# Kernel tuning notes

Hardware: AMD Instinct MI355X
Metric: run time of the kernel (lower is better)

The kernel has to match this reference:

```python
import jax, jax.numpy as jnp
import numpy as np

B, N, C, H, HD, HH, WW, K, ALPHA = 8, 4096, 256, 8, 32, 64, 64, 5, 4.0


def setup_inputs() -> dict:
    key = jax.random.key(0)
    ks = jax.random.split(key, 6)
    return {
        "x": jax.random.normal(ks[0], (B, N, C), jnp.float32),
        "W_qg": jax.random.normal(ks[1], (C, 2 * C), jnp.float32) * 0.02,
        "W_kv": jax.random.normal(ks[2], (C, 2 * C), jnp.float32) * 0.02,
        "W_proj": jax.random.normal(ks[3], (C, C), jnp.float32) * 0.02,
        "b_proj": jnp.zeros((C,), jnp.float32),
        "dwc_w": jax.random.normal(ks[4], (HD, 1, K, K), jnp.float32) * 0.05,
        "dwc_b": jnp.zeros((HD,), jnp.float32),
        "power_p": jnp.zeros((1, H, 1, HD), jnp.float32),
    }


def _safe_pow(x, p):
    # x >= 0 (post-relu). 0**p == 0 for p > 0; guard base so grads stay finite.
    xs = jnp.where(x > 0, x, 1.0)
    return jnp.where(x > 0, xs ** p, 0.0)


def reference(x, W_qg, W_kv, W_proj, b_proj, dwc_w, dwc_b, power_p):
    qg = x @ W_qg                                  # (B,N,2C)
    q, g = qg[..., :C], qg[..., C:]
    kv = x @ W_kv                                  # (B,N,2C)
    k = kv[..., :C].reshape(B, N, H, HD).transpose(0, 2, 1, 3)   # (B,H,N,hd)
    v = kv[..., C:].reshape(B, N, H, HD).transpose(0, 2, 1, 3)
    q = q.reshape(B, N, H, HD).transpose(0, 2, 1, 3)

    power = 1.0 + ALPHA * jax.nn.sigmoid(power_p)  # (1,H,1,hd)
    # x_s = q_pos@kv_s + q_neg@kv_s = (q_pos+q_neg)@kv_s, kv_s = (k_pos+k_neg)^T v_s
    q_sum = _safe_pow(jax.nn.relu(q), power) + _safe_pow(jax.nn.relu(-q), power)
    k_sum = _safe_pow(jax.nn.relu(k), power) + _safe_pow(jax.nn.relu(-k), power)

    v_s, v_o = v[..., : HD // 2], v[..., HD // 2 :]
    kv_s = jnp.einsum('bhnd,bhne->bhde', k_sum, v_s)
    kv_o = jnp.einsum('bhnd,bhne->bhde', k_sum, v_o)
    x_s = jnp.einsum('bhnd,bhde->bhne', q_sum, kv_s)
    x_o = jnp.einsum('bhnd,bhde->bhne', q_sum, kv_o)
    x_att = jnp.concatenate([x_s, x_o], -1).transpose(0, 2, 1, 3).reshape(B, N, C)

    # depthwise conv branch: exact layout replication of torch permute/reshape chain
    v_img = v.transpose(0, 2, 1, 3).reshape(B * H, HD, HH, WW)
    pad = K // 2
    v_loc = jax.lax.conv_general_dilated(
        v_img, dwc_w, (1, 1), [(pad, pad), (pad, pad)],
        feature_group_count=HD,
        dimension_numbers=('NCHW', 'OIHW', 'NCHW')) + dwc_b[None, :, None, None]
    v_loc = v_loc.reshape(B, H, HD, N).transpose(0, 2, 1, 3).reshape(B, C, N).transpose(0, 2, 1)

    return ((x_att + v_loc) * g) @ W_proj + b_proj
```

## Files before the change

### kernel.cpp

```cpp
#include <hip/hip_runtime.h>
#include <hip/hip_bf16.h>
#include <math.h>

#define B_ 8
#define N_ 4096
#define C_ 256
#define H_ 8
#define HD_ 32
#define BN_ (B_ * N_)
#define E_ ((size_t)BN_ * C_)

typedef __attribute__((ext_vector_type(8))) short short8;
typedef __attribute__((ext_vector_type(4))) float f32x4;

__device__ __forceinline__ float b2f(__hip_bfloat16 x) { return __bfloat162float(x); }

__device__ __forceinline__ void gl_lds16(const void* gp, void* lp) {
    __builtin_amdgcn_global_load_lds(
        (const __attribute__((address_space(1))) unsigned int*)gp,
        (__attribute__((address_space(3))) unsigned int*)lp,
        16, 0, 0);
}

__device__ __forceinline__ float fast_abspow(float v, float p) {
    float av = fabsf(v);
    return (av > 0.f) ? __builtin_amdgcn_exp2f(p * __builtin_amdgcn_logf(av)) : 0.f;
}

__device__ __forceinline__ float bf_lo(unsigned u) { return __uint_as_float(u << 16); }
__device__ __forceinline__ float bf_hi(unsigned u) { return __uint_as_float(u & 0xffff0000u); }
__device__ __forceinline__ unsigned short f2bfbits(float f) {
    __hip_bfloat16 h = __float2bfloat16(f);
    return *(unsigned short*)&h;
}
__device__ __forceinline__ unsigned pack2(float lo, float hi) {
    return (unsigned)f2bfbits(lo) | ((unsigned)f2bfbits(hi) << 16);
}

__global__ __launch_bounds__(256) void cvt_all(
    const float* __restrict__ x, const float* __restrict__ Wqg,
    const float* __restrict__ Wkv, const float* __restrict__ Wp,
    const float* __restrict__ pp,
    __hip_bfloat16* __restrict__ xb, __hip_bfloat16* __restrict__ Wt1,
    __hip_bfloat16* __restrict__ Wt2, float* __restrict__ powers,
    float* __restrict__ kv_mat2)
{
    int t = threadIdx.x;
    int bid0 = blockIdx.x;
    if (bid0 < 4096) {
        size_t i = ((size_t)bid0 * 256 + t) * 8;
        float4 a = *(const float4*)&x[i];
        float4 b = *(const float4*)&x[i + 4];
        uint4 o = {pack2(a.x, a.y), pack2(a.z, a.w), pack2(b.x, b.y), pack2(b.z, b.w)};
        *(uint4*)&xb[i] = o;
        return;
    }
    int bid = bid0 - 4096;
    if (bid == 80) {
        powers[t] = 1.0f + 4.0f / (1.0f + expf(-pp[t]));
        return;
    }
    if (bid >= 81) {
        ((float4*)kv_mat2)[(size_t)(bid - 81) * 256 + t] = (float4){0.f, 0.f, 0.f, 0.f};
        return;
    }
    __shared__ float tile[64][65];
    const float* src;
    __hip_bfloat16* dst;
    int scols, tr, tc, dn0;
    if (bid < 32)      { src = Wqg; scols = 512; tr = bid >> 3;        tc = bid & 7;        dst = Wt1; dn0 = tc * 64; }
    else if (bid < 64) { src = Wkv; scols = 512; tr = (bid - 32) >> 3; tc = (bid - 32) & 7; dst = Wt1; dn0 = 512 + tc * 64; }
    else               { src = Wp;  scols = 256; tr = (bid - 64) >> 2; tc = (bid - 64) & 3; dst = Wt2; dn0 = tc * 64; }
    int tx = t & 63, ty = t >> 6;
    #pragma unroll
    for (int i = 0; i < 16; i++) {
        int r = ty + i * 4;
        tile[r][tx] = src[(size_t)(tr * 64 + r) * scols + tc * 64 + tx];
    }
    __syncthreads();
    #pragma unroll
    for (int i = 0; i < 16; i++) {
        int n_local = ty + i * 4;
        dst[(size_t)(dn0 + n_local) * 256 + tr * 64 + tx] = __float2bfloat16(tile[tx][n_local]);
    }
}

__global__ __launch_bounds__(256) void gemm1_mfma(
    const __hip_bfloat16* __restrict__ xb, const __hip_bfloat16* __restrict__ Wt1,
    const float* __restrict__ powers,
    __hip_bfloat16* __restrict__ q16, __hip_bfloat16* __restrict__ k16,
    __hip_bfloat16* __restrict__ g16, __hip_bfloat16* __restrict__ v16)
{
    __shared__ __align__(16) unsigned short ABs[128 * 128];
    int t = threadIdx.x;
    int w = t >> 6, l = t & 63;
    int bswz = (blockIdx.x & 7) * 256 + (blockIdx.x >> 3);
    int row0 = (bswz >> 3) * 128;
    int colb = bswz & 7;
    int col0 = colb * 128;
    int wm = (w >> 1) * 64, wn = (w & 1) * 64;
    int lane15 = l & 15, quad = l >> 4;
    int srow4 = l >> 2;
    int sgc = ((l & 3) ^ ((l >> 3) & 3)) * 8;

    f32x4 acc[4][4];
    #pragma unroll
    for (int mi = 0; mi < 4; mi++)
        #pragma unroll
        for (int ni = 0; ni < 4; ni++) acc[mi][ni] = (f32x4){0.f, 0.f, 0.f, 0.f};

    #pragma unroll
    for (int j = 0; j < 2; j++) {
        int rowl = j * 64 + w * 16 + srow4;
        gl_lds16(&xb[(size_t)(row0 + rowl) * 256 + sgc],
                 &ABs[(j * 64 + w * 16) * 32]);
        gl_lds16(&Wt1[(size_t)(col0 + rowl) * 256 + sgc],
                 &ABs[8192 + (j * 64 + w * 16) * 32]);
    }
    __syncthreads();

    for (int ti = 0; ti < 8; ti++) {
        int cur = ti & 1;
        if (ti < 7) {
            int nxt = cur ^ 1;
            int kn = (ti + 1) * 32;
            #pragma unroll
            for (int j = 0; j < 2; j++) {
                int rowl = j * 64 + w * 16 + srow4;
                gl_lds16(&xb[(size_t)(row0 + rowl) * 256 + kn + sgc],
                         &ABs[nxt * 4096 + (j * 64 + w * 16) * 32]);
                gl_lds16(&Wt1[(size_t)(col0 + rowl) * 256 + kn + sgc],
                         &ABs[8192 + nxt * 4096 + (j * 64 + w * 16) * 32]);
            }
        }
        const unsigned short* Ac = ABs + cur * 4096;
        const unsigned short* Bc = ABs + 8192 + cur * 4096;
        short8 a[4], b[4];
        #pragma unroll
        for (int mi = 0; mi < 4; mi++) {
            int r = wm + mi * 16 + lane15;
            a[mi] = *(const short8*)&Ac[r * 32 + ((quad ^ ((r >> 1) & 3)) << 3)];
        }
        #pragma unroll
        for (int ni = 0; ni < 4; ni++) {
            int r = wn + ni * 16 + lane15;
            b[ni] = *(const short8*)&Bc[r * 32 + ((quad ^ ((r >> 1) & 3)) << 3)];
        }
        #pragma unroll
        for (int mi = 0; mi < 4; mi++)
            #pragma unroll
            for (int ni = 0; ni < 4; ni++)
                acc[mi][ni] = __builtin_amdgcn_mfma_f32_16x16x32_bf16(a[mi], b[ni], acc[mi][ni], 0, 0, 0);
        __syncthreads();
    }

    int region = colb >> 1;
    bool dopow = (region == 0) || (region == 2);
    __hip_bfloat16* dst = (region == 0) ? q16 : (region == 1) ? g16 : (region == 2) ? k16 : v16;
    int cbase = col0 & 255;
    #pragma unroll
    for (int mi = 0; mi < 4; mi++) {
        #pragma unroll
        for (int ni = 0; ni < 4; ni++) {
            int rowb = wm + mi * 16 + quad * 4;
            int coll = wn + ni * 16 + lane15;
            float p = powers[cbase + coll];
            int cchunk = coll >> 3, cin = coll & 7;
            #pragma unroll
            for (int r = 0; r < 4; r++) {
                int rl = rowb + r;
                float v = acc[mi][ni][r];
                float o = dopow ? fast_abspow(v, p) : v;
                ABs[rl * 128 + ((cchunk ^ (rl & 15)) << 3) + cin] = f2bfbits(o);
            }
        }
    }
    __syncthreads();
    #pragma unroll
    for (int j = 0; j < 8; j++) {
        int g = j * 256 + t;
        int rl = g >> 4, chunk = g & 15;
        uint4 vv = *(const uint4*)&ABs[rl * 128 + ((chunk ^ (rl & 15)) << 3)];
        *(uint4*)&dst[(size_t)(row0 + rl) * 256 + cbase + chunk * 8] = vv;
    }
}

__global__ __launch_bounds__(256) void kvconv_kernel(
    const __hip_bfloat16* __restrict__ k16, const __hip_bfloat16* __restrict__ v16,
    float* __restrict__ kv_mat2,
    const float* __restrict__ w, const float* __restrict__ bias,
    __hip_bfloat16* __restrict__ vloc)
{
    __shared__ __align__(16) unsigned char smraw[18560];
    int t = threadIdx.x;

    if (blockIdx.x < 512) {
        unsigned short (*KV)[32][136] = (unsigned short (*)[32][136])smraw;
        int w_ = t >> 6, l = t & 63;
        int lane15 = l & 15, quad = l >> 4;
        int bid = blockIdx.x;
        int pair = bid >> 3, seg = bid & 7;
        int b = pair >> 3, h = pair & 7;
        int nloc = t & 127, cs = (t >> 7) * 16;

        f32x4 acc[2][2];
        #pragma unroll
        for (int di = 0; di < 2; di++)
            #pragma unroll
            for (int ei = 0; ei < 2; ei++) acc[di][ei] = (f32x4){0.f, 0.f, 0.f, 0.f};

        const size_t base = (size_t)b * N_ * 256 + h * 32 + cs;
        for (int c4 = 0; c4 < 4; c4++) {
            int n0 = seg * 512 + c4 * 128;
            const uint4* kp = (const uint4*)(k16 + base + (size_t)(n0 + nloc) * 256);
            uint4 ka = kp[0], kb = kp[1];
            const uint4* vp = (const uint4*)(v16 + base + (size_t)(n0 + nloc) * 256);
            uint4 va = vp[0], vb = vp[1];
            __syncthreads();
            unsigned kw[8] = {ka.x, ka.y, ka.z, ka.w, kb.x, kb.y, kb.z, kb.w};
            unsigned vw[8] = {va.x, va.y, va.z, va.w, vb.x, vb.y, vb.z, vb.w};
            #pragma unroll
            for (int j = 0; j < 8; j++) {
                KV[0][cs + 2 * j][nloc]     = (unsigned short)(kw[j] & 0xffffu);
                KV[0][cs + 2 * j + 1][nloc] = (unsigned short)(kw[j] >> 16);
                KV[1][cs + 2 * j][nloc]     = (unsigned short)(vw[j] & 0xffffu);
                KV[1][cs + 2 * j + 1][nloc] = (unsigned short)(vw[j] >> 16);
            }
            __syncthreads();
            int nb = w_ * 32 + quad * 8;
            short8 a[2], bb[2];
            #pragma unroll
            for (int di = 0; di < 2; di++)
                a[di] = *(const short8*)&KV[0][di * 16 + lane15][nb];
            #pragma unroll
            for (int ei = 0; ei < 2; ei++)
                bb[ei] = *(const short8*)&KV[1][ei * 16 + lane15][nb];
            #pragma unroll
            for (int di = 0; di < 2; di++)
                #pragma unroll
                for (int ei = 0; ei < 2; ei++)
                    acc[di][ei] = __builtin_amdgcn_mfma_f32_16x16x32_bf16(a[di], bb[ei], acc[di][ei], 0, 0, 0);
        }

        __syncthreads();
        float* red = (float*)smraw;
        #pragma unroll
        for (int di = 0; di < 2; di++)
            #pragma unroll
            for (int ei = 0; ei < 2; ei++) {
                int e = ei * 16 + lane15;
                #pragma unroll
                for (int r = 0; r < 4; r++) {
                    int d = di * 16 + quad * 4 + r;
                    red[w_ * 1056 + e * 33 + d] = acc[di][ei][r];
                }
            }
        __syncthreads();
        #pragma unroll
        for (int j = 0; j < 4; j++) {
            int o = j * 256 + t;
            int e = o >> 5, d = o & 31;
            float s = red[e * 33 + d] + red[1056 + e * 33 + d]
                    + red[2112 + e * 33 + d] + red[3168 + e * 33 + d];
            atomicAdd(&kv_mat2[(size_t)b * 8192 + e * 256 + h * 32 + d], s);
        }
        return;
    }

    float* img = (float*)smraw;
    float* wl  = (float*)(smraw + 18432);
    int gid = blockIdx.x - 512;
    int DD = gid & 31;
    if (t < 128) {
        int row = t >> 1, side = (t & 1) * 68;
        *(float4*)&img[row * 72 + side] = (float4){0.f, 0.f, 0.f, 0.f};
    }
    if (t < 25) wl[t] = w[DD * 25 + t];
    {
        int row = t >> 2, colb = (t & 3) * 16;
        const uint4* src = (const uint4*)(v16 + (size_t)gid * 4096 + row * 64 + colb);
        uint4 u0 = src[0], u1 = src[1];
        float4* d = (float4*)&img[row * 72 + 4 + colb];
        d[0] = (float4){bf_lo(u0.x), bf_hi(u0.x), bf_lo(u0.y), bf_hi(u0.y)};
        d[1] = (float4){bf_lo(u0.z), bf_hi(u0.z), bf_lo(u0.w), bf_hi(u0.w)};
        d[2] = (float4){bf_lo(u1.x), bf_hi(u1.x), bf_lo(u1.y), bf_hi(u1.y)};
        d[3] = (float4){bf_lo(u1.z), bf_hi(u1.z), bf_lo(u1.w), bf_hi(u1.w)};
    }
    __syncthreads();
    float bs = bias[DD];
    int x0 = (t & 15) * 4, yb = t >> 4;
    #pragma unroll
    for (int s = 0; s < 4; s++) {
        int y = yb + s * 16;
        float a0 = bs, a1 = bs, a2 = bs, a3 = bs;
        #pragma unroll
        for (int ky = 0; ky < 5; ky++) {
            int row = y + ky - 2;
            if (row < 0 || row >= 64) continue;
            const float* rp = &img[row * 72 + x0];
            float4 w0 = *(const float4*)rp;
            float4 w1 = *(const float4*)(rp + 4);
            float4 w2 = *(const float4*)(rp + 8);
            float win[12] = {w0.x, w0.y, w0.z, w0.w, w1.x, w1.y, w1.z, w1.w,
                             w2.x, w2.y, w2.z, w2.w};
            #pragma unroll
            for (int kx = 0; kx < 5; kx++) {
                float wt = wl[ky * 5 + kx];
                a0 += wt * win[2 + kx];
                a1 += wt * win[3 + kx];
                a2 += wt * win[4 + kx];
                a3 += wt * win[5 + kx];
            }
        }
        unsigned lo = pack2(a0, a1);
        unsigned hi = pack2(a2, a3);
        *(uint2*)(vloc + (size_t)gid * 4096 + y * 64 + x0) = (uint2){lo, hi};
    }
}

#define A2P 264
__global__ __launch_bounds__(512) void att_gemm2(
    const __hip_bfloat16* __restrict__ q16, const float* __restrict__ kv_mat2,
    const __hip_bfloat16* __restrict__ vloc, const __hip_bfloat16* __restrict__ g16,
    const __hip_bfloat16* __restrict__ Wt2, const float* __restrict__ bp,
    float* __restrict__ out)
{
    __shared__ __align__(16) unsigned short QA[64 * A2P];
    __shared__ __align__(16) unsigned short Bs[256 * 32];
    int t = threadIdx.x;
    int w = t >> 6, l = t & 63;
    int r0 = blockIdx.x * 64;
    int b = r0 >> 12, n0 = r0 & 4095;
    int lane15 = l & 15, quad = l >> 4;
    int h = w;

    {
        const uint4* qsrc = (const uint4*)(q16 + (size_t)(r0 + (t >> 3)) * 256 + (t & 7) * 32);
        uint4* qdst = (uint4*)&QA[(t >> 3) * A2P + (t & 7) * 32];
        #pragma unroll
        for (int j = 0; j < 4; j++) qdst[j] = qsrc[j];
    }
    __syncthreads();

    short8 afr[4];
    #pragma unroll
    for (int m = 0; m < 4; m++)
        afr[m] = *(const short8*)&QA[(m * 16 + lane15) * A2P + h * 32 + quad * 8];

    short8 bfr[2];
    #pragma unroll
    for (int nt = 0; nt < 2; nt++) {
        const float4* kp = (const float4*)(kv_mat2 + (size_t)b * 8192 +
            (size_t)(nt * 16 + lane15) * 256 + h * 32 + quad * 8);
        float4 ka = kp[0], kb = kp[1];
        short8 bb;
        bb[0] = (short)f2bfbits(ka.x); bb[1] = (short)f2bfbits(ka.y);
        bb[2] = (short)f2bfbits(ka.z); bb[3] = (short)f2bfbits(ka.w);
        bb[4] = (short)f2bfbits(kb.x); bb[5] = (short)f2bfbits(kb.y);
        bb[6] = (short)f2bfbits(kb.z); bb[7] = (short)f2bfbits(kb.w);
        bfr[nt] = bb;
    }

    f32x4 ac[4][2];
    #pragma unroll
    for (int m = 0; m < 4; m++)
        #pragma unroll
        for (int nt = 0; nt < 2; nt++)
            ac[m][nt] = __builtin_amdgcn_mfma_f32_16x16x32_bf16(
                afr[m], bfr[nt], (f32x4){0.f, 0.f, 0.f, 0.f}, 0, 0, 0);

    #pragma unroll
    for (int m = 0; m < 4; m++) {
        #pragma unroll
        for (int nt = 0; nt < 2; nt++) {
            int col = h * 32 + nt * 16 + lane15;
            int rowb = m * 16 + quad * 4;
            size_t img = ((size_t)((b * 8 + (col & 7)) * 32 + (col >> 3))) * 4096 + n0 + rowb;
            uint2 vv = *(const uint2*)(vloc + img);
            float vl[4] = {bf_lo(vv.x), bf_hi(vv.x), bf_lo(vv.y), bf_hi(vv.y)};
            #pragma unroll
            for (int i = 0; i < 4; i++) {
                float gg = b2f(g16[(size_t)(r0 + rowb + i) * 256 + col]);
                float val = (ac[m][nt][i] + vl[i]) * gg;
                QA[(rowb + i) * A2P + col] = f2bfbits(val);
            }
        }
    }

    int wm = (w & 1) * 32, wn = (w >> 1) * 64;
    f32x4 acc2[2][4];
    #pragma unroll
    for (int mi = 0; mi < 2; mi++)
        #pragma unroll
        for (int ni = 0; ni < 4; ni++) acc2[mi][ni] = (f32x4){0.f, 0.f, 0.f, 0.f};

    for (int k0 = 0; k0 < 256; k0 += 32) {
        __syncthreads();
        #pragma unroll
        for (int j = 0; j < 2; j++) {
            int rowl = j * 128 + w * 16 + (l >> 2);
            int gchunk = (l & 3) ^ ((rowl >> 1) & 3);
            gl_lds16(&Wt2[(size_t)rowl * 256 + k0 + gchunk * 8],
                     &Bs[(j * 128 + w * 16) * 32]);
        }
        __syncthreads();
        short8 a[2], bb[4];
        #pragma unroll
        for (int mi = 0; mi < 2; mi++)
            a[mi] = *(const short8*)&QA[(wm + mi * 16 + lane15) * A2P + k0 + quad * 8];
        #pragma unroll
        for (int ni = 0; ni < 4; ni++) {
            int r = wn + ni * 16 + lane15;
            bb[ni] = *(const short8*)&Bs[r * 32 + ((quad ^ ((r >> 1) & 3)) << 3)];
        }
        #pragma unroll
        for (int mi = 0; mi < 2; mi++)
            #pragma unroll
            for (int ni = 0; ni < 4; ni++)
                acc2[mi][ni] = __builtin_amdgcn_mfma_f32_16x16x32_bf16(a[mi], bb[ni], acc2[mi][ni], 0, 0, 0);
    }

    #pragma unroll
    for (int mi = 0; mi < 2; mi++) {
        #pragma unroll
        for (int ni = 0; ni < 4; ni++) {
            int row = r0 + wm + mi * 16 + quad * 4;
            int col = wn + ni * 16 + lane15;
            float bv = bp[col];
            #pragma unroll
            for (int r = 0; r < 4; r++)
                out[(size_t)(row + r) * 256 + col] = acc2[mi][ni][r] + bv;
        }
    }
}

extern "C" void kernel_launch(void* const* d_in, const int* in_sizes, int n_in,
                              void* d_out, int out_size, void* d_ws, size_t ws_size,
                              hipStream_t stream) {
    const float* x      = (const float*)d_in[0];
    const float* W_qg   = (const float*)d_in[1];
    const float* W_kv   = (const float*)d_in[2];
    const float* W_proj = (const float*)d_in[3];
    const float* b_proj = (const float*)d_in[4];
    const float* dwc_w  = (const float*)d_in[5];
    const float* dwc_b  = (const float*)d_in[6];
    const float* pow_p  = (const float*)d_in[7];
    float* out = (float*)d_out;

    float* ws = (float*)d_ws;
    const size_t E = E_;
    __hip_bfloat16* q16  = (__hip_bfloat16*)ws;
    __hip_bfloat16* k16  = (__hip_bfloat16*)(ws + E / 2);
    __hip_bfloat16* g16  = (__hip_bfloat16*)(ws + E);
    __hip_bfloat16* v16  = (__hip_bfloat16*)(ws + 3 * E / 2);
    __hip_bfloat16* xb   = (__hip_bfloat16*)(ws + 2 * E);
    __hip_bfloat16* vl16 = (__hip_bfloat16*)(ws + 5 * E / 2);
    float* kv_mat2 = ws + 3 * E;
    __hip_bfloat16* Wt1 = (__hip_bfloat16*)(kv_mat2 + 65536);
    __hip_bfloat16* Wt2 = Wt1 + 262144;
    float* powers = (float*)(Wt2 + 65536);

    cvt_all<<<4096 + 81 + 64, 256, 0, stream>>>(x, W_qg, W_kv, W_proj, pow_p, xb, Wt1, Wt2, powers, kv_mat2);
    gemm1_mfma<<<2048, 256, 0, stream>>>(xb, Wt1, powers, q16, k16, g16, v16);
    kvconv_kernel<<<512 + 2048, 256, 0, stream>>>(k16, v16, kv_mat2, dwc_w, dwc_b, vl16);
    att_gemm2<<<512, 512, 0, stream>>>(q16, kv_mat2, vl16, g16, Wt2, b_proj, out);
}
```

Before: 171.1 us.

## Widen gemm1 tile to 128x256 with K-step 64, single-buffered

```diff
diff --git a/kernel.cpp b/kernel.cpp
--- a/kernel.cpp
+++ b/kernel.cpp
@@ -91,97 +91,93 @@
     __hip_bfloat16* __restrict__ q16, __hip_bfloat16* __restrict__ k16,
     __hip_bfloat16* __restrict__ g16, __hip_bfloat16* __restrict__ v16)
 {
-    __shared__ __align__(16) unsigned short ABs[128 * 128];
+    __shared__ __align__(16) unsigned short ABs[128 * 64 + 256 * 64];
+    unsigned short* As = ABs;
+    unsigned short* Bs = ABs + 128 * 64;
     int t = threadIdx.x;
     int w = t >> 6, l = t & 63;
-    int bswz = (blockIdx.x & 7) * 256 + (blockIdx.x >> 3);
-    int row0 = (bswz >> 3) * 128;
-    int colb = bswz & 7;
-    int col0 = colb * 128;
-    int wm = (w >> 1) * 64, wn = (w & 1) * 64;
+    int bswz = (blockIdx.x & 7) * 128 + (blockIdx.x >> 3);
+    int row0 = (bswz >> 2) * 128;
+    int cp = bswz & 3;
+    int col0 = cp * 256;
+    int wm = (w >> 1) * 64, wn = (w & 1) * 128;
     int lane15 = l & 15, quad = l >> 4;
-    int srow4 = l >> 2;
-    int sgc = ((l & 3) ^ ((l >> 3) & 3)) * 8;
-
-    f32x4 acc[4][4];
+    int sr8 = l >> 3;
+    int sc = ((l & 7) ^ sr8) * 8;
+    int r7 = lane15 & 7;
+
+    f32x4 acc[4][8];
     #pragma unroll
     for (int mi = 0; mi < 4; mi++)
         #pragma unroll
-        for (int ni = 0; ni < 4; ni++) acc[mi][ni] = (f32x4){0.f, 0.f, 0.f, 0.f};
-
-    #pragma unroll
-    for (int j = 0; j < 2; j++) {
-        int rowl = j * 64 + w * 16 + srow4;
-        gl_lds16(&xb[(size_t)(row0 + rowl) * 256 + sgc],
-                 &ABs[(j * 64 + w * 16) * 32]);
-        gl_lds16(&Wt1[(size_t)(col0 + rowl) * 256 + sgc],
-                 &ABs[8192 + (j * 64 + w * 16) * 32]);
-    }
-    __syncthreads();
-
-    for (int ti = 0; ti < 8; ti++) {
-        int cur = ti & 1;
-        if (ti < 7) {
-            int nxt = cur ^ 1;
-            int kn = (ti + 1) * 32;
-            #pragma unroll
-            for (int j = 0; j < 2; j++) {
-                int rowl = j * 64 + w * 16 + srow4;
-                gl_lds16(&xb[(size_t)(row0 + rowl) * 256 + kn + sgc],
-                         &ABs[nxt * 4096 + (j * 64 + w * 16) * 32]);
-                gl_lds16(&Wt1[(size_t)(col0 + rowl) * 256 + kn + sgc],
-                         &ABs[8192 + nxt * 4096 + (j * 64 + w * 16) * 32]);
+        for (int ni = 0; ni < 8; ni++) acc[mi][ni] = (f32x4){0.f, 0.f, 0.f, 0.f};
+
+    for (int k0 = 0; k0 < 256; k0 += 64) {
+        #pragma unroll
+        for (int j = 0; j < 4; j++) {
+            int rowl = j * 32 + w * 8 + sr8;
+            gl_lds16(&xb[(size_t)(row0 + rowl) * 256 + k0 + sc],
+                     &As[(j * 32 + w * 8) * 64]);
+        }
+        #pragma unroll
+        for (int j = 0; j < 8; j++) {
+            int rowl = j * 32 + w * 8 + sr8;
+            gl_lds16(&Wt1[(size_t)(col0 + rowl) * 256 + k0 + sc],
+                     &Bs[(j * 32 + w * 8) * 64]);
+        }
+        __syncthreads();
+        #pragma unroll
+        for (int kh = 0; kh < 2; kh++) {
+            int cs_k = ((kh * 4 + quad) ^ r7) * 8;
+            short8 a[4], b[8];
+            #pragma unroll
+            for (int mi = 0; mi < 4; mi++)
+                a[mi] = *(const short8*)&As[(wm + mi * 16 + lane15) * 64 + cs_k];
+            #pragma unroll
+            for (int ni = 0; ni < 8; ni++)
+                b[ni] = *(const short8*)&Bs[(wn + ni * 16 + lane15) * 64 + cs_k];
+            #pragma unroll
+            for (int mi = 0; mi < 4; mi++)
+                #pragma unroll
+                for (int ni = 0; ni < 8; ni++)
+                    acc[mi][ni] = __builtin_amdgcn_mfma_f32_16x16x32_bf16(a[mi], b[ni], acc[mi][ni], 0, 0, 0);
+        }
+        __syncthreads();
+    }
+
+    bool dopow = (cp == 0) || (cp == 2);
+    __hip_bfloat16* dst = (cp == 0) ? q16 : (cp == 1) ? g16 : (cp == 2) ? k16 : v16;
+    #pragma unroll
+    for (int ch = 0; ch < 2; ch++) {
+        if ((w & 1) == ch) {
+            #pragma unroll
+            for (int mi = 0; mi < 4; mi++) {
+                #pragma unroll
+                for (int ni = 0; ni < 8; ni++) {
+                    int rowb = wm + mi * 16 + quad * 4;
+                    int collF = wn + ni * 16 + lane15;
+                    int coll = collF - ch * 128;
+                    float p = powers[collF];
+                    int cchunk = coll >> 3, cin = coll & 7;
+                    #pragma unroll
+                    for (int r = 0; r < 4; r++) {
+                        int rl = rowb + r;
+                        float v = acc[mi][ni][r];
+                        float o = dopow ? fast_abspow(v, p) : v;
+                        ABs[rl * 128 + ((cchunk ^ (rl & 15)) << 3) + cin] = f2bfbits(o);
+                    }
+                }
             }
         }
-        const unsigned short* Ac = ABs + cur * 4096;
-        const unsigned short* Bc = ABs + 8192 + cur * 4096;
-        short8 a[4], b[4];
-        #pragma unroll
-        for (int mi = 0; mi < 4; mi++) {
-            int r = wm + mi * 16 + lane15;
-            a[mi] = *(const short8*)&Ac[r * 32 + ((quad ^ ((r >> 1) & 3)) << 3)];
-        }
-        #pragma unroll
-        for (int ni = 0; ni < 4; ni++) {
-            int r = wn + ni * 16 + lane15;
-            b[ni] = *(const short8*)&Bc[r * 32 + ((quad ^ ((r >> 1) & 3)) << 3)];
-        }
-        #pragma unroll
-        for (int mi = 0; mi < 4; mi++)
-            #pragma unroll
-            for (int ni = 0; ni < 4; ni++)
-                acc[mi][ni] = __builtin_amdgcn_mfma_f32_16x16x32_bf16(a[mi], b[ni], acc[mi][ni], 0, 0, 0);
-        __syncthreads();
-    }
-
-    int region = colb >> 1;
-    bool dopow = (region == 0) || (region == 2);
-    __hip_bfloat16* dst = (region == 0) ? q16 : (region == 1) ? g16 : (region == 2) ? k16 : v16;
-    int cbase = col0 & 255;
-    #pragma unroll
-    for (int mi = 0; mi < 4; mi++) {
-        #pragma unroll
-        for (int ni = 0; ni < 4; ni++) {
-            int rowb = wm + mi * 16 + quad * 4;
-            int coll = wn + ni * 16 + lane15;
-            float p = powers[cbase + coll];
-            int cchunk = coll >> 3, cin = coll & 7;
-            #pragma unroll
-            for (int r = 0; r < 4; r++) {
-                int rl = rowb + r;
-                float v = acc[mi][ni][r];
-                float o = dopow ? fast_abspow(v, p) : v;
-                ABs[rl * 128 + ((cchunk ^ (rl & 15)) << 3) + cin] = f2bfbits(o);
-            }
-        }
-    }
-    __syncthreads();
-    #pragma unroll
-    for (int j = 0; j < 8; j++) {
-        int g = j * 256 + t;
-        int rl = g >> 4, chunk = g & 15;
-        uint4 vv = *(const uint4*)&ABs[rl * 128 + ((chunk ^ (rl & 15)) << 3)];
-        *(uint4*)&dst[(size_t)(row0 + rl) * 256 + cbase + chunk * 8] = vv;
+        __syncthreads();
+        #pragma unroll
+        for (int j = 0; j < 8; j++) {
+            int g = j * 256 + t;
+            int rl = g >> 4, chunk = g & 15;
+            uint4 vv = *(const uint4*)&ABs[rl * 128 + ((chunk ^ (rl & 15)) << 3)];
+            *(uint4*)&dst[(size_t)(row0 + rl) * 256 + ch * 128 + chunk * 8] = vv;
+        }
+        __syncthreads();
     }
 }
 
@@ -461,7 +457,7 @@
     float* powers = (float*)(Wt2 + 65536);
 
     cvt_all<<<4096 + 81 + 64, 256, 0, stream>>>(x, W_qg, W_kv, W_proj, pow_p, xb, Wt1, Wt2, powers, kv_mat2);
-    gemm1_mfma<<<2048, 256, 0, stream>>>(xb, Wt1, powers, q16, k16, g16, v16);
+    gemm1_mfma<<<1024, 256, 0, stream>>>(xb, Wt1, powers, q16, k16, g16, v16);
     kvconv_kernel<<<512 + 2048, 256, 0, stream>>>(k16, v16, kv_mat2, dwc_w, dwc_b, vl16);
     att_gemm2<<<512, 512, 0, stream>>>(q16, kv_mat2, vl16, g16, Wt2, b_proj, out);
 }
```

Result: slower. 235.6 us (+37.7%).

## Replace double-buffered BK=32 GEMM1 loop with single-buffered BK=64 tiles

Applied to the files above, without the earlier changes.

```diff
diff --git a/kernel.cpp b/kernel.cpp
--- a/kernel.cpp
+++ b/kernel.cpp
@@ -92,6 +92,8 @@
     __hip_bfloat16* __restrict__ g16, __hip_bfloat16* __restrict__ v16)
 {
     __shared__ __align__(16) unsigned short ABs[128 * 128];
+    unsigned short* As = ABs;
+    unsigned short* Bs = ABs + 128 * 64;
     int t = threadIdx.x;
     int w = t >> 6, l = t & 63;
     int bswz = (blockIdx.x & 7) * 256 + (blockIdx.x >> 3);
@@ -100,8 +102,9 @@
     int col0 = colb * 128;
     int wm = (w >> 1) * 64, wn = (w & 1) * 64;
     int lane15 = l & 15, quad = l >> 4;
-    int srow4 = l >> 2;
-    int sgc = ((l & 3) ^ ((l >> 3) & 3)) * 8;
+    int sr8 = l >> 3;
+    int sc = ((l & 7) ^ sr8) * 8;
+    int r7 = lane15 & 7;
 
     f32x4 acc[4][4];
     #pragma unroll
@@ -109,48 +112,32 @@
         #pragma unroll
         for (int ni = 0; ni < 4; ni++) acc[mi][ni] = (f32x4){0.f, 0.f, 0.f, 0.f};
 
-    #pragma unroll
-    for (int j = 0; j < 2; j++) {
-        int rowl = j * 64 + w * 16 + srow4;
-        gl_lds16(&xb[(size_t)(row0 + rowl) * 256 + sgc],
-                 &ABs[(j * 64 + w * 16) * 32]);
-        gl_lds16(&Wt1[(size_t)(col0 + rowl) * 256 + sgc],
-                 &ABs[8192 + (j * 64 + w * 16) * 32]);
-    }
-    __syncthreads();
-
-    for (int ti = 0; ti < 8; ti++) {
-        int cur = ti & 1;
-        if (ti < 7) {
-            int nxt = cur ^ 1;
-            int kn = (ti + 1) * 32;
-            #pragma unroll
-            for (int j = 0; j < 2; j++) {
-                int rowl = j * 64 + w * 16 + srow4;
-                gl_lds16(&xb[(size_t)(row0 + rowl) * 256 + kn + sgc],
-                         &ABs[nxt * 4096 + (j * 64 + w * 16) * 32]);
-                gl_lds16(&Wt1[(size_t)(col0 + rowl) * 256 + kn + sgc],
-                         &ABs[8192 + nxt * 4096 + (j * 64 + w * 16) * 32]);
-            }
-        }
-        const unsigned short* Ac = ABs + cur * 4096;
-        const unsigned short* Bc = ABs + 8192 + cur * 4096;
-        short8 a[4], b[4];
-        #pragma unroll
-        for (int mi = 0; mi < 4; mi++) {
-            int r = wm + mi * 16 + lane15;
-            a[mi] = *(const short8*)&Ac[r * 32 + ((quad ^ ((r >> 1) & 3)) << 3)];
-        }
-        #pragma unroll
-        for (int ni = 0; ni < 4; ni++) {
-            int r = wn + ni * 16 + lane15;
-            b[ni] = *(const short8*)&Bc[r * 32 + ((quad ^ ((r >> 1) & 3)) << 3)];
-        }
-        #pragma unroll
-        for (int mi = 0; mi < 4; mi++)
+    for (int k0 = 0; k0 < 256; k0 += 64) {
+        #pragma unroll
+        for (int j = 0; j < 4; j++) {
+            int rowl = j * 32 + w * 8 + sr8;
+            gl_lds16(&xb[(size_t)(row0 + rowl) * 256 + k0 + sc],
+                     &As[(j * 32 + w * 8) * 64]);
+            gl_lds16(&Wt1[(size_t)(col0 + rowl) * 256 + k0 + sc],
+                     &Bs[(j * 32 + w * 8) * 64]);
+        }
+        __syncthreads();
+        #pragma unroll
+        for (int kh = 0; kh < 2; kh++) {
+            int cs_k = ((kh * 4 + quad) ^ r7) * 8;
+            short8 a[4], b[4];
+            #pragma unroll
+            for (int mi = 0; mi < 4; mi++)
+                a[mi] = *(const short8*)&As[(wm + mi * 16 + lane15) * 64 + cs_k];
             #pragma unroll
             for (int ni = 0; ni < 4; ni++)
-                acc[mi][ni] = __builtin_amdgcn_mfma_f32_16x16x32_bf16(a[mi], b[ni], acc[mi][ni], 0, 0, 0);
+                b[ni] = *(const short8*)&Bs[(wn + ni * 16 + lane15) * 64 + cs_k];
+            #pragma unroll
+            for (int mi = 0; mi < 4; mi++)
+                #pragma unroll
+                for (int ni = 0; ni < 4; ni++)
+                    acc[mi][ni] = __builtin_amdgcn_mfma_f32_16x16x32_bf16(a[mi], b[ni], acc[mi][ni], 0, 0, 0);
+        }
         __syncthreads();
     }
 
```

Measured after the change: 169.7 us. No clear change (-0.8%).
